# Kernel tuning notes

Hardware: AMD Instinct MI355X
Metric: run time of the kernel (lower is better)

The kernel has to match this reference:

```python
import jax, jax.numpy as jnp
import numpy as np

NUM_HEADS = 64
DIM = 128
# Rotation schedule: all (i, j) with i < j in row-major order, matching
# GivensRotationPerHead._create_rotation_indices. R = DIM*(DIM-1)//2 = 8128.
_II, _JJ = np.triu_indices(DIM, k=1)


def setup_inputs() -> dict:
    key = jax.random.key(0)
    thetas = jax.random.normal(key, (NUM_HEADS, _II.shape[0]), dtype=jnp.float32) * 0.01
    return {
        "thetas": thetas,
        "rot_i": jnp.asarray(_II, dtype=jnp.int32),
        "rot_j": jnp.asarray(_JJ, dtype=jnp.int32),
    }


def reference(thetas, rot_i, rot_j):
    # thetas: [H, R]; rot_i, rot_j: [R]
    H, R = thetas.shape
    dim = DIM
    # Precompute all cos/sin once ([R, H, 1]) instead of per-step trig.
    c = jnp.cos(thetas.T)[:, :, None]
    s = jnp.sin(thetas.T)[:, :, None]
    Q0 = jnp.broadcast_to(jnp.eye(dim, dtype=thetas.dtype), (H, dim, dim))

    def body(Q, xs):
        i, j, ci, si = xs
        Qi = Q[:, i, :]  # [H, dim]
        Qj = Q[:, j, :]  # [H, dim]
        Q = Q.at[:, i, :].set(ci * Qi + si * Qj)
        Q = Q.at[:, j, :].set(-si * Qi + ci * Qj)
        return Q, None

    Q, _ = jax.lax.scan(body, Q0, (rot_i, rot_j, c, s))
    return Q
```

## Files before the change

### kernel.cpp

```cpp
#include <hip/hip_runtime.h>

#define DIM 128
#define NHEAD 64
#define NROT 8128
#define NSEG28 28
#define MHEAD28 57344
#define KAC 168
#define CSROWS 64

typedef float f4 __attribute__((ext_vector_type(4)));
typedef short bf8 __attribute__((ext_vector_type(8)));
typedef unsigned short u16;

__device__ const int S_A0[NSEG28] = {0,0,0,8,8,8,16,16,16,24,24,32,32,40,40,
                                     48,48,56,56,64,64,72,80,88,96,104,112,120};
__device__ const int S_J0[NSEG28] = {8,56,104,16,64,112,24,72,120,32,80,40,88,48,96,
                                     56,104,64,112,72,120,80,88,96,104,112,120,128};
__device__ const int S_NJ[NSEG28] = {48,48,24,48,48,16,48,48,8,48,48,48,40,48,32,
                                     48,24,48,16,48,8,48,40,32,24,16,8,0};
__device__ const int S_OFF[NSEG28] = {0,3136,6272,7296,10432,13568,14144,17280,20416,
                                      20672,23808,26944,30080,32384,35520,37120,40256,
                                      41280,44416,44992,48128,48384,51520,53824,55424,
                                      56448,57024,57280};
__device__ const int S_INTRA[NSEG28] = {1,0,0,1,0,0,1,0,0,1,0,1,0,1,0,
                                        1,0,1,0,1,0,1,1,1,1,1,1,1};

__device__ __forceinline__ void sincos_poly(float x, float& sn, float& cn) {
    float x2 = x * x;
    sn = x * fmaf(x2, fmaf(x2, 8.33333333e-3f, -1.66666667e-1f), 1.0f);
    cn = fmaf(x2, fmaf(x2, 4.16666667e-2f, -0.5f), 1.0f);
}

__device__ __forceinline__ u16 f2bf(float v) {
    unsigned b = __float_as_uint(v);
    b += 0x7FFF + ((b >> 16) & 1);
    return (u16)(b >> 16);
}
__device__ __forceinline__ float bf2f(u16 h) {
    return __uint_as_float(((unsigned)h) << 16);
}

struct Row { f4 q0, q1, q2, q3; };

__device__ __forceinline__ void ldrow_u(Row& R, const float* p) {
    const f4* c4 = (const f4*)p;
    R.q0 = c4[0]; R.q1 = c4[1]; R.q2 = c4[2]; R.q3 = c4[3];
}

__device__ __forceinline__ float rowv(const Row& R, float p[8], float v) {
#define ROT2(c, s, T) { float pv = p[T]; float nv = fmaf((c), v, -((s) * pv)); \
                        p[T] = fmaf((s), v, (c) * pv); v = nv; }
    ROT2(R.q0.x, R.q0.y, 0) ROT2(R.q0.z, R.q0.w, 1)
    ROT2(R.q1.x, R.q1.y, 2) ROT2(R.q1.z, R.q1.w, 3)
    ROT2(R.q2.x, R.q2.y, 4) ROT2(R.q2.z, R.q2.w, 5)
    ROT2(R.q3.x, R.q3.y, 6) ROT2(R.q3.z, R.q3.w, 7)
#undef ROT2
    return v;
}

__device__ __forceinline__ void store_bf(u16* oh, u16* ol, int idx, float v, bool act) {
    u16 h = f2bf(v);
    u16 l = f2bf(v - bf2f(h));
    if (act) { oh[idx] = h; ol[idx] = l; }
}

__global__ __launch_bounds__(64, 1)
void chain28(const float* __restrict__ th_all,
             u16* __restrict__ MhW, u16* __restrict__ MlW)
{
    __shared__ __align__(16) float csx[56 + 48 * 16];

    const int lane = threadIdx.x;
    const int head = blockIdx.x & 63;
    const int s    = blockIdx.x >> 6;
    const int a0 = S_A0[s], j0 = S_J0[s], nj = S_NJ[s], n = 8 + nj;
    const bool intra = S_INTRA[s] != 0;
    const float* __restrict__ th = th_all + head * NROT;
    u16* __restrict__ oh = MhW + (size_t)head * MHEAD28 + S_OFF[s];
    u16* __restrict__ ol = MlW + (size_t)head * MHEAD28 + S_OFF[s];
    const bool cact = lane < n;
    const int ne = 8 * nj;
    const int d1 = j0 - a0 - 1;

    float thx[6];
    #pragma unroll
    for (int it = 0; it < 6; ++it) {
        if (it * 64 < ne) {
            int e = lane + it * 64;
            int t = e & 7, jr = e >> 3;
            int i = a0 + t;
            thx[it] = th[((i * (255 - i)) >> 1) + d1 - t + jr];
        }
    }
    float thi = 0.0f;
    if (intra && lane < 28) {
        int t1 = 0, rem = lane;
        while (rem >= 7 - t1) { rem -= 7 - t1; ++t1; }
        int t2 = t1 + 1 + rem;
        int i  = a0 + t1;
        thi = th[((i * (255 - i)) >> 1) + (t2 - t1 - 1)];
    }
    #pragma unroll
    for (int it = 0; it < 6; ++it) {
        if (it * 64 < ne) {
            int e = lane + it * 64;
            float sn, cn; sincos_poly(thx[it], sn, cn);
            csx[56 + 2 * e] = cn; csx[56 + 2 * e + 1] = sn;
        }
    }
    if (intra && lane < 28) {
        float sn, cn; sincos_poly(thi, sn, cn);
        csx[2 * lane] = cn; csx[2 * lane + 1] = sn;
    }
    __syncthreads();

    float p[8];
    #pragma unroll
    for (int t = 0; t < 8; ++t) p[t] = (lane == t) ? 1.0f : 0.0f;

    if (intra) {
        int idx = 0;
        #pragma unroll
        for (int t1 = 0; t1 < 8; ++t1) {
            #pragma unroll
            for (int t2 = t1 + 1; t2 < 8; ++t2) {
                float c = csx[2 * idx], sn = csx[2 * idx + 1];
                float pa = p[t1];
                p[t1] = fmaf(c, pa,    sn * p[t2]);
                p[t2] = fmaf(c, p[t2], -(sn * pa));
                ++idx;
            }
        }
    }

    if (nj > 0) {
        const float* cs = csx + 56;
        const int jv = lane - 8;
        Row A0, A1, B0, B1;
        ldrow_u(A0, cs); ldrow_u(A1, cs + 16);
        #pragma unroll 1
        for (int r = 0; r < nj; r += 4) {
            ldrow_u(B0, cs + 16 * (r + 2)); ldrow_u(B1, cs + 16 * (r + 3));
            float v0 = rowv(A0, p, (r     == jv) ? 1.0f : 0.0f);
            float v1 = rowv(A1, p, (r + 1 == jv) ? 1.0f : 0.0f);
            store_bf(oh, ol, (8 + r)     * n + lane, v0, cact);
            store_bf(oh, ol, (8 + r + 1) * n + lane, v1, cact);
            if (r + 4 < nj) { ldrow_u(A0, cs + 16 * (r + 4));
                              ldrow_u(A1, cs + 16 * (r + 5)); }
            float v2 = rowv(B0, p, (r + 2 == jv) ? 1.0f : 0.0f);
            float v3 = rowv(B1, p, (r + 3 == jv) ? 1.0f : 0.0f);
            store_bf(oh, ol, (8 + r + 2) * n + lane, v2, cact);
            store_bf(oh, ol, (8 + r + 3) * n + lane, v3, cact);
        }
    }

    #pragma unroll
    for (int t = 0; t < 8; ++t)
        store_bf(oh, ol, t * n + lane, p[t], cact);
}

__global__ __launch_bounds__(256, 1)
void compose4w(const u16* __restrict__ MhA, const u16* __restrict__ MlA,
               float* __restrict__ out)
{
    __shared__ u16 AhT[16][KAC];
    __shared__ u16 AlT[16][KAC];

    const int tid  = threadIdx.x;
    const int lane = tid & 63;
    const int w    = tid >> 6;
    const int head = blockIdx.x & 63;
    const int sl   = blockIdx.x >> 6;
    const int c0   = sl * 16;
    const u16* __restrict__ Mh = MhA + (size_t)head * MHEAD28;
    const u16* __restrict__ Ml = MlA + (size_t)head * MHEAD28;

    {
        int c = tid & 15, rr = tid >> 4, cg = c0 + c;
        for (int k = DIM + rr; k < KAC; k += 16) { AhT[c][k] = 0; AlT[c][k] = 0; }
        for (int r = rr; r < DIM; r += 16) {
            u16 h, l;
            if (r < 56 && cg < 56) { h = Mh[r * 56 + cg]; l = Ml[r * 56 + cg]; }
            else                   { h = (r == cg) ? (u16)0x3F80 : (u16)0; l = 0; }
            AhT[c][r] = h; AlT[c][r] = l;
        }
    }
    __syncthreads();

    const int fr = lane & 15;
    const int fk = (lane >> 4) * 8;
    const int r4 = (lane >> 4) * 4;
    const int ro = 16 * w;

    auto ldM = [&](int s, bf8& ah0, bf8& al0, bf8& ah1, bf8& al1) {
        const int n = 8 + S_NJ[s];
        const u16* __restrict__ Msh = Mh + S_OFF[s];
        const u16* __restrict__ Msl = Ml + S_OFF[s];
        const int rA  = ro + fr;
        const int rAc = (rA < n) ? rA : (n - 1);
        const int kc0 = (fk <= n - 8) ? fk : (n - 8);
        const int kx  = 32 + fk;
        const int kc1 = (kx <= n - 8) ? kx : (n - 8);
        ah0 = *(const bf8*)&Msh[(size_t)rAc * n + kc0];
        al0 = *(const bf8*)&Msl[(size_t)rAc * n + kc0];
        ah1 = *(const bf8*)&Msh[(size_t)rAc * n + kc1];
        al1 = *(const bf8*)&Msl[(size_t)rAc * n + kc1];
    };

    bf8 cah0, cal0, cah1, cal1;
    bf8 nah0, nal0, nah1, nal1;
    ldM(1, cah0, cal0, cah1, cal1);

    #pragma unroll 1
    for (int s = 1; s < NSEG28; ++s) {
        const int a0 = S_A0[s], j0 = S_J0[s], n = 8 + S_NJ[s];

        const int kk0 = fk, kx = 32 + fk;
        const int b0 = (kk0 < 8) ? (a0 + kk0) : ((kk0 < n) ? (j0 + kk0 - 8) : 128);
        const int b1 = (kx  < 8) ? (a0 + kx)  : ((kx  < n) ? (j0 + kx  - 8) : 128);
        bf8 bh0 = *(const bf8*)&AhT[fr][b0];
        bf8 bl0 = *(const bf8*)&AlT[fr][b0];
        bf8 bh1 = *(const bf8*)&AhT[fr][b1];
        bf8 bl1 = *(const bf8*)&AlT[fr][b1];

        if (s + 1 < NSEG28) ldM(s + 1, nah0, nal0, nah1, nal1);

        const bool act = ro < n;
        f4 acc = {0, 0, 0, 0};
        if (act) {
            acc = __builtin_amdgcn_mfma_f32_16x16x32_bf16(cah0, bh0, acc, 0, 0, 0);
            acc = __builtin_amdgcn_mfma_f32_16x16x32_bf16(cah0, bl0, acc, 0, 0, 0);
            acc = __builtin_amdgcn_mfma_f32_16x16x32_bf16(cal0, bh0, acc, 0, 0, 0);
            acc = __builtin_amdgcn_mfma_f32_16x16x32_bf16(cal0, bl0, acc, 0, 0, 0);
            acc = __builtin_amdgcn_mfma_f32_16x16x32_bf16(cah1, bh1, acc, 0, 0, 0);
            acc = __builtin_amdgcn_mfma_f32_16x16x32_bf16(cah1, bl1, acc, 0, 0, 0);
            acc = __builtin_amdgcn_mfma_f32_16x16x32_bf16(cal1, bh1, acc, 0, 0, 0);
            acc = __builtin_amdgcn_mfma_f32_16x16x32_bf16(cal1, bl1, acc, 0, 0, 0);
        }

        __syncthreads();

        const int rowq = ro + r4;
        if (act && rowq < n) {
            const int rg = (rowq < 8) ? (a0 + rowq) : (j0 + rowq - 8);
            float v0 = acc[0], v1 = acc[1], v2 = acc[2], v3 = acc[3];
            u16 h0 = f2bf(v0), h1 = f2bf(v1), h2 = f2bf(v2), h3 = f2bf(v3);
            u16 l0 = f2bf(v0 - bf2f(h0)), l1 = f2bf(v1 - bf2f(h1));
            u16 l2 = f2bf(v2 - bf2f(h2)), l3 = f2bf(v3 - bf2f(h3));
            ushort4 hv; hv.x = h0; hv.y = h1; hv.z = h2; hv.w = h3;
            ushort4 lv; lv.x = l0; lv.y = l1; lv.z = l2; lv.w = l3;
            *(ushort4*)&AhT[fr][rg] = hv;
            *(ushort4*)&AlT[fr][rg] = lv;
        }
        __syncthreads();

        cah0 = nah0; cal0 = nal0; cah1 = nah1; cal1 = nal1;
    }

    {
        int c = tid & 15, rr = tid >> 4;
        float* o = out + (size_t)head * (DIM * DIM) + c0;
        for (int r = rr; r < DIM; r += 16)
            o[r * DIM + c] = bf2f(AhT[c][r]) + bf2f(AlT[c][r]);
    }
}

#define QA(r, c) Q[(r)][ (c) ^ ((r) & 31) ]
#define ROTP(c, s, T, v) { float pt = p[T]; p[T] = fmaf((c), pt, (s) * (v)); \
                           (v) = fmaf((c), (v), -((s) * pt)); }
__device__ __forceinline__ void rot8q(const Row& r, float p[8], float& v) {
    ROTP(r.q0.x, r.q0.y, 0, v) ROTP(r.q0.z, r.q0.w, 1, v)
    ROTP(r.q1.x, r.q1.y, 2, v) ROTP(r.q1.z, r.q1.w, 3, v)
    ROTP(r.q2.x, r.q2.y, 4, v) ROTP(r.q2.z, r.q2.w, 5, v)
    ROTP(r.q3.x, r.q3.y, 6, v) ROTP(r.q3.z, r.q3.w, 7, v)
}

__global__ __launch_bounds__(64, 1)
void chain_mono(const float* __restrict__ th_all, float* __restrict__ outp)
{
    __shared__ float Q[DIM][64];
    __shared__ __align__(16) float csx[56 + CSROWS * 16];

    const int lane = threadIdx.x;
    const int head = blockIdx.x & 63;
    const int cb   = blockIdx.x >> 6;
    const int col_glob = cb * 64 + lane;
    const float* __restrict__ th = th_all + head * NROT;

    for (int r = 0; r < DIM; ++r)
        QA(r, lane) = (r == col_glob) ? 1.0f : 0.0f;

    #pragma unroll 1
    for (int g = 0; g < 16; ++g) {
        const int a0  = 8 * g;
        const int ntr = 120 - a0;
        float p[8];
        const int nsub = (ntr > CSROWS) ? 2 : 1;
        #pragma unroll 1
        for (int sub = 0; sub < nsub; ++sub) {
            const int r0 = sub * CSROWS;
            const int nr = (ntr - r0) < CSROWS ? (ntr - r0) : CSROWS;
            const int ne = 8 * nr;
            __syncthreads();
            float thx[8];
            #pragma unroll
            for (int it = 0; it < 8; ++it) {
                if (it * 64 < ne) {
                    int e = lane + it * 64;
                    int t = e & 7, jr = r0 + (e >> 3);
                    int i = a0 + t;
                    thx[it] = th[((i * (255 - i)) >> 1) + jr + 7 - t];
                }
            }
            float thi = 0.0f;
            if (sub == 0 && lane < 28) {
                int t1 = 0, rem = lane;
                while (rem >= 7 - t1) { rem -= 7 - t1; ++t1; }
                int t2 = t1 + 1 + rem;
                int i  = a0 + t1;
                thi = th[((i * (255 - i)) >> 1) + (t2 - t1 - 1)];
            }
            #pragma unroll
            for (int it = 0; it < 8; ++it) {
                if (it * 64 < ne) {
                    int e = lane + it * 64;
                    float sn, cn; sincos_poly(thx[it], sn, cn);
                    csx[56 + 2 * e] = cn; csx[56 + 2 * e + 1] = sn;
                }
            }
            if (sub == 0 && lane < 28) {
                float sn, cn; sincos_poly(thi, sn, cn);
                csx[2 * lane] = cn; csx[2 * lane + 1] = sn;
            }
            __syncthreads();

            if (sub == 0) {
                #pragma unroll
                for (int t = 0; t < 8; ++t) p[t] = QA(a0 + t, lane);
                int idx = 0;
                #pragma unroll
                for (int t1 = 0; t1 < 8; ++t1) {
                    #pragma unroll
                    for (int t2 = t1 + 1; t2 < 8; ++t2) {
                        float c = csx[2 * idx], sn = csx[2 * idx + 1];
                        float pa = p[t1];
                        p[t1] = fmaf(c, pa,    sn * p[t2]);
                        p[t2] = fmaf(c, p[t2], -(sn * pa));
                        ++idx;
                    }
                }
            }
            if (nr > 0) {
                const float* cs = csx + 56;
                const int base = a0 + 8 + r0;
                Row A0, A1, B0, B1;
                float vA0, vA1, vB0, vB1;
                auto ldpair = [&](Row& R, float& v, int r) {
                    ldrow_u(R, cs + 16 * r);
                    v = QA(base + r, lane);
                };
                ldpair(A0, vA0, 0); ldpair(A1, vA1, 1);
                #pragma unroll 1
                for (int r = 0; r < nr; r += 4) {
                    ldpair(B0, vB0, r + 2); ldpair(B1, vB1, r + 3);
                    rot8q(A0, p, vA0); rot8q(A1, p, vA1);
                    QA(base + r, lane)     = vA0;
                    QA(base + r + 1, lane) = vA1;
                    if (r + 4 < nr) { ldpair(A0, vA0, r + 4); ldpair(A1, vA1, r + 5); }
                    rot8q(B0, p, vB0); rot8q(B1, p, vB1);
                    QA(base + r + 2, lane) = vB0;
                    QA(base + r + 3, lane) = vB1;
                }
            }
        }
        #pragma unroll
        for (int t = 0; t < 8; ++t) QA(a0 + t, lane) = p[t];
    }

    __syncthreads();
    float* o = outp + head * (DIM * DIM) + col_glob;
    #pragma unroll 1
    for (int r = 0; r < DIM; ++r) o[r * DIM] = QA(r, lane);
}

extern "C" void kernel_launch(void* const* d_in, const int* in_sizes, int n_in,
                              void* d_out, int out_size, void* d_ws, size_t ws_size,
                              hipStream_t stream) {
    const float* thetas = (const float*)d_in[0];
    float* out = (float*)d_out;
    const size_t need = (size_t)NHEAD * MHEAD28 * 2 * sizeof(u16);

    if (ws_size >= need) {
        u16* MhW = (u16*)d_ws;
        u16* MlW = MhW + (size_t)NHEAD * MHEAD28;
        chain28<<<dim3(NSEG28 * NHEAD), dim3(64), 0, stream>>>(thetas, MhW, MlW);
        compose4w<<<dim3(8 * NHEAD), dim3(256), 0, stream>>>(MhW, MlW, out);
    } else {
        chain_mono<<<dim3(2 * NHEAD), dim3(64), 0, stream>>>(thetas, out);
    }
}
```

Baseline: 40.96 us.

## Coarsen Givens chain segmentation from 28 eight-row segments to 7 thirty-two-row segments

```diff
diff --git a/kernel.cpp b/kernel.cpp
--- a/kernel.cpp
+++ b/kernel.cpp
@@ -3,8 +3,8 @@
 #define DIM 128
 #define NHEAD 64
 #define NROT 8128
-#define NSEG28 28
-#define MHEAD28 57344
+#define NSEG7 7
+#define MHEAD7 25600
 #define KAC 168
 #define CSROWS 64
 
@@ -12,18 +12,12 @@
 typedef short bf8 __attribute__((ext_vector_type(8)));
 typedef unsigned short u16;
 
-__device__ const int S_A0[NSEG28] = {0,0,0,8,8,8,16,16,16,24,24,32,32,40,40,
-                                     48,48,56,56,64,64,72,80,88,96,104,112,120};
-__device__ const int S_J0[NSEG28] = {8,56,104,16,64,112,24,72,120,32,80,40,88,48,96,
-                                     56,104,64,112,72,120,80,88,96,104,112,120,128};
-__device__ const int S_NJ[NSEG28] = {48,48,24,48,48,16,48,48,8,48,48,48,40,48,32,
-                                     48,24,48,16,48,8,48,40,32,24,16,8,0};
-__device__ const int S_OFF[NSEG28] = {0,3136,6272,7296,10432,13568,14144,17280,20416,
-                                      20672,23808,26944,30080,32384,35520,37120,40256,
-                                      41280,44416,44992,48128,48384,51520,53824,55424,
-                                      56448,57024,57280};
-__device__ const int S_INTRA[NSEG28] = {1,0,0,1,0,0,1,0,0,1,0,1,0,1,0,
-                                        1,0,1,0,1,0,1,1,1,1,1,1,1};
+__device__ const int C_A0[NSEG7]   = {0,0,0,32,32,64,96};
+__device__ const int C_J0[NSEG7]   = {32,64,96,64,96,96,128};
+__device__ const int C_NJ[NSEG7]   = {32,32,32,32,32,32,0};
+__device__ const int C_N[NSEG7]    = {64,64,64,64,64,64,32};
+__device__ const int C_OFF[NSEG7]  = {0,4096,8192,12288,16384,20480,24576};
+__device__ const int C_INTRA[NSEG7]= {1,0,0,1,0,1,1};
 
 __device__ __forceinline__ void sincos_poly(float x, float& sn, float& cn) {
     float x2 = x * x;
@@ -40,22 +34,8 @@
     return __uint_as_float(((unsigned)h) << 16);
 }
 
-struct Row { f4 q0, q1, q2, q3; };
-
-__device__ __forceinline__ void ldrow_u(Row& R, const float* p) {
-    const f4* c4 = (const f4*)p;
-    R.q0 = c4[0]; R.q1 = c4[1]; R.q2 = c4[2]; R.q3 = c4[3];
-}
-
-__device__ __forceinline__ float rowv(const Row& R, float p[8], float v) {
-#define ROT2(c, s, T) { float pv = p[T]; float nv = fmaf((c), v, -((s) * pv)); \
-                        p[T] = fmaf((s), v, (c) * pv); v = nv; }
-    ROT2(R.q0.x, R.q0.y, 0) ROT2(R.q0.z, R.q0.w, 1)
-    ROT2(R.q1.x, R.q1.y, 2) ROT2(R.q1.z, R.q1.w, 3)
-    ROT2(R.q2.x, R.q2.y, 4) ROT2(R.q2.z, R.q2.w, 5)
-    ROT2(R.q3.x, R.q3.y, 6) ROT2(R.q3.z, R.q3.w, 7)
-#undef ROT2
-    return v;
+__device__ __forceinline__ int tri_base(int i) {
+    return (i * (2 * DIM - 1 - i)) >> 1;
 }
 
 __device__ __forceinline__ void store_bf(u16* oh, u16* ol, int idx, float v, bool act) {
@@ -65,66 +45,75 @@
 }
 
 __global__ __launch_bounds__(64, 1)
-void chain28(const float* __restrict__ th_all,
-             u16* __restrict__ MhW, u16* __restrict__ MlW)
+void chain7(const float* __restrict__ th_all,
+            u16* __restrict__ MhW, u16* __restrict__ MlW)
 {
-    __shared__ __align__(16) float csx[56 + 48 * 16];
+    __shared__ __align__(16) float csx[992 + 32 * 64];
 
     const int lane = threadIdx.x;
     const int head = blockIdx.x & 63;
     const int s    = blockIdx.x >> 6;
-    const int a0 = S_A0[s], j0 = S_J0[s], nj = S_NJ[s], n = 8 + nj;
-    const bool intra = S_INTRA[s] != 0;
+    const int a0 = C_A0[s], j0 = C_J0[s], nj = C_NJ[s], n = C_N[s];
+    const bool intra = C_INTRA[s] != 0;
     const float* __restrict__ th = th_all + head * NROT;
-    u16* __restrict__ oh = MhW + (size_t)head * MHEAD28 + S_OFF[s];
-    u16* __restrict__ ol = MlW + (size_t)head * MHEAD28 + S_OFF[s];
+    u16* __restrict__ oh = MhW + (size_t)head * MHEAD7 + C_OFF[s];
+    u16* __restrict__ ol = MlW + (size_t)head * MHEAD7 + C_OFF[s];
     const bool cact = lane < n;
-    const int ne = 8 * nj;
+    const int ne = 32 * nj;
     const int d1 = j0 - a0 - 1;
 
-    float thx[6];
-    #pragma unroll
-    for (int it = 0; it < 6; ++it) {
+    float thx[16];
+    #pragma unroll
+    for (int it = 0; it < 16; ++it) {
         if (it * 64 < ne) {
             int e = lane + it * 64;
-            int t = e & 7, jr = e >> 3;
-            int i = a0 + t;
-            thx[it] = th[((i * (255 - i)) >> 1) + d1 - t + jr];
-        }
-    }
-    float thi = 0.0f;
-    if (intra && lane < 28) {
-        int t1 = 0, rem = lane;
-        while (rem >= 7 - t1) { rem -= 7 - t1; ++t1; }
-        int t2 = t1 + 1 + rem;
-        int i  = a0 + t1;
-        thi = th[((i * (255 - i)) >> 1) + (t2 - t1 - 1)];
-    }
-    #pragma unroll
-    for (int it = 0; it < 6; ++it) {
+            int t = e & 31, r = e >> 5;
+            thx[it] = th[tri_base(a0 + t) + d1 + r - t];
+        }
+    }
+    float thi[8];
+    #pragma unroll
+    for (int it = 0; it < 8; ++it) {
+        int e = lane + it * 64;
+        if (intra && e < 496) {
+            int t1 = 0, rem = e;
+            while (rem >= 31 - t1) { rem -= 31 - t1; ++t1; }
+            int t2 = t1 + 1 + rem;
+            thi[it] = th[tri_base(a0 + t1) + (t2 - t1 - 1)];
+        }
+    }
+    #pragma unroll
+    for (int it = 0; it < 16; ++it) {
         if (it * 64 < ne) {
             int e = lane + it * 64;
             float sn, cn; sincos_poly(thx[it], sn, cn);
-            csx[56 + 2 * e] = cn; csx[56 + 2 * e + 1] = sn;
-        }
-    }
-    if (intra && lane < 28) {
-        float sn, cn; sincos_poly(thi, sn, cn);
-        csx[2 * lane] = cn; csx[2 * lane + 1] = sn;
+            csx[992 + 2 * e] = cn; csx[992 + 2 * e + 1] = sn;
+        }
+    }
+    #pragma unroll
+    for (int it = 0; it < 8; ++it) {
+        int e = lane + it * 64;
+        if (intra && e < 496) {
+            float sn, cn; sincos_poly(thi[it], sn, cn);
+            csx[2 * e] = cn; csx[2 * e + 1] = sn;
+        }
     }
     __syncthreads();
 
-    float p[8];
-    #pragma unroll
-    for (int t = 0; t < 8; ++t) p[t] = (lane == t) ? 1.0f : 0.0f;
+    float p[32];
+    #pragma unroll
+    for (int t = 0; t < 32; ++t) p[t] = (lane == t) ? 1.0f : 0.0f;
 
     if (intra) {
+        f4 cc;
         int idx = 0;
         #pragma unroll
-        for (int t1 = 0; t1 < 8; ++t1) {
-            #pragma unroll
-            for (int t2 = t1 + 1; t2 < 8; ++t2) {
-                float c = csx[2 * idx], sn = csx[2 * idx + 1];
+        for (int t1 = 0; t1 < 31; ++t1) {
+            #pragma unroll
+            for (int t2 = t1 + 1; t2 < 32; ++t2) {
+                float c, sn;
+                if ((idx & 1) == 0) { cc = *(const f4*)&csx[2 * idx]; c = cc.x; sn = cc.y; }
+                else                { c = cc.z; sn = cc.w; }
                 float pa = p[t1];
                 p[t1] = fmaf(c, pa,    sn * p[t2]);
                 p[t2] = fmaf(c, p[t2], -(sn * pa));
@@ -134,34 +123,35 @@
     }
 
     if (nj > 0) {
-        const float* cs = csx + 56;
-        const int jv = lane - 8;
-        Row A0, A1, B0, B1;
-        ldrow_u(A0, cs); ldrow_u(A1, cs + 16);
-        #pragma unroll 1
-        for (int r = 0; r < nj; r += 4) {
-            ldrow_u(B0, cs + 16 * (r + 2)); ldrow_u(B1, cs + 16 * (r + 3));
-            float v0 = rowv(A0, p, (r     == jv) ? 1.0f : 0.0f);
-            float v1 = rowv(A1, p, (r + 1 == jv) ? 1.0f : 0.0f);
-            store_bf(oh, ol, (8 + r)     * n + lane, v0, cact);
-            store_bf(oh, ol, (8 + r + 1) * n + lane, v1, cact);
-            if (r + 4 < nj) { ldrow_u(A0, cs + 16 * (r + 4));
-                              ldrow_u(A1, cs + 16 * (r + 5)); }
-            float v2 = rowv(B0, p, (r + 2 == jv) ? 1.0f : 0.0f);
-            float v3 = rowv(B1, p, (r + 3 == jv) ? 1.0f : 0.0f);
-            store_bf(oh, ol, (8 + r + 2) * n + lane, v2, cact);
-            store_bf(oh, ol, (8 + r + 3) * n + lane, v3, cact);
-        }
-    }
-
-    #pragma unroll
-    for (int t = 0; t < 8; ++t)
+        const float* cs = csx + 992;
+        const int jv = lane - 32;
+        #pragma unroll 2
+        for (int r = 0; r < nj; ++r) {
+            const f4* c4 = (const f4*)(cs + r * 64);
+            f4 q[16];
+            #pragma unroll
+            for (int i = 0; i < 16; ++i) q[i] = c4[i];
+            float v = (r == jv) ? 1.0f : 0.0f;
+            #pragma unroll
+            for (int t = 0; t < 32; t += 2) {
+                f4 qq = q[t >> 1];
+                { float pv = p[t];     float nv = fmaf(qq.x, v, -(qq.y * pv));
+                  p[t]     = fmaf(qq.y, v, qq.x * pv); v = nv; }
+                { float pv = p[t + 1]; float nv = fmaf(qq.z, v, -(qq.w * pv));
+                  p[t + 1] = fmaf(qq.w, v, qq.z * pv); v = nv; }
+            }
+            store_bf(oh, ol, (32 + r) * n + lane, v, cact);
+        }
+    }
+
+    #pragma unroll
+    for (int t = 0; t < 32; ++t)
         store_bf(oh, ol, t * n + lane, p[t], cact);
 }
 
 __global__ __launch_bounds__(256, 1)
-void compose4w(const u16* __restrict__ MhA, const u16* __restrict__ MlA,
-               float* __restrict__ out)
+void compose7(const u16* __restrict__ MhA, const u16* __restrict__ MlA,
+              float* __restrict__ out)
 {
     __shared__ u16 AhT[16][KAC];
     __shared__ u16 AlT[16][KAC];
@@ -172,15 +162,15 @@
     const int head = blockIdx.x & 63;
     const int sl   = blockIdx.x >> 6;
     const int c0   = sl * 16;
-    const u16* __restrict__ Mh = MhA + (size_t)head * MHEAD28;
-    const u16* __restrict__ Ml = MlA + (size_t)head * MHEAD28;
+    const u16* __restrict__ Mh = MhA + (size_t)head * MHEAD7;
+    const u16* __restrict__ Ml = MlA + (size_t)head * MHEAD7;
 
     {
         int c = tid & 15, rr = tid >> 4, cg = c0 + c;
         for (int k = DIM + rr; k < KAC; k += 16) { AhT[c][k] = 0; AlT[c][k] = 0; }
         for (int r = rr; r < DIM; r += 16) {
             u16 h, l;
-            if (r < 56 && cg < 56) { h = Mh[r * 56 + cg]; l = Ml[r * 56 + cg]; }
+            if (r < 64 && cg < 64) { h = Mh[r * 64 + cg]; l = Ml[r * 64 + cg]; }
             else                   { h = (r == cg) ? (u16)0x3F80 : (u16)0; l = 0; }
             AhT[c][r] = h; AlT[c][r] = l;
         }
@@ -193,37 +183,35 @@
     const int ro = 16 * w;
 
     auto ldM = [&](int s, bf8& ah0, bf8& al0, bf8& ah1, bf8& al1) {
-        const int n = 8 + S_NJ[s];
-        const u16* __restrict__ Msh = Mh + S_OFF[s];
-        const u16* __restrict__ Msl = Ml + S_OFF[s];
+        const int n = C_N[s];
+        const u16* __restrict__ Msh = Mh + C_OFF[s];
+        const u16* __restrict__ Msl = Ml + C_OFF[s];
         const int rA  = ro + fr;
         const int rAc = (rA < n) ? rA : (n - 1);
-        const int kc0 = (fk <= n - 8) ? fk : (n - 8);
         const int kx  = 32 + fk;
         const int kc1 = (kx <= n - 8) ? kx : (n - 8);
-        ah0 = *(const bf8*)&Msh[(size_t)rAc * n + kc0];
-        al0 = *(const bf8*)&Msl[(size_t)rAc * n + kc0];
+        ah0 = *(const bf8*)&Msh[(size_t)rAc * n + fk];
+        al0 = *(const bf8*)&Msl[(size_t)rAc * n + fk];
         ah1 = *(const bf8*)&Msh[(size_t)rAc * n + kc1];
         al1 = *(const bf8*)&Msl[(size_t)rAc * n + kc1];
     };
 
-    bf8 cah0, cal0, cah1, cal1;
-    bf8 nah0, nal0, nah1, nal1;
+    bf8 cah0, cal0, cah1, cal1, nah0, nal0, nah1, nal1;
     ldM(1, cah0, cal0, cah1, cal1);
 
     #pragma unroll 1
-    for (int s = 1; s < NSEG28; ++s) {
-        const int a0 = S_A0[s], j0 = S_J0[s], n = 8 + S_NJ[s];
-
-        const int kk0 = fk, kx = 32 + fk;
-        const int b0 = (kk0 < 8) ? (a0 + kk0) : ((kk0 < n) ? (j0 + kk0 - 8) : 128);
-        const int b1 = (kx  < 8) ? (a0 + kx)  : ((kx  < n) ? (j0 + kx  - 8) : 128);
+    for (int s = 1; s < NSEG7; ++s) {
+        const int a0 = C_A0[s], j0 = C_J0[s], n = C_N[s];
+
+        const int kx = 32 + fk;
+        const int b0 = a0 + fk;
+        const int b1 = (kx < n) ? (j0 + fk) : 128;
         bf8 bh0 = *(const bf8*)&AhT[fr][b0];
         bf8 bl0 = *(const bf8*)&AlT[fr][b0];
         bf8 bh1 = *(const bf8*)&AhT[fr][b1];
         bf8 bl1 = *(const bf8*)&AlT[fr][b1];
 
-        if (s + 1 < NSEG28) ldM(s + 1, nah0, nal0, nah1, nal1);
+        if (s + 1 < NSEG7) ldM(s + 1, nah0, nal0, nah1, nal1);
 
         const bool act = ro < n;
         f4 acc = {0, 0, 0, 0};
@@ -242,7 +230,7 @@
 
         const int rowq = ro + r4;
         if (act && rowq < n) {
-            const int rg = (rowq < 8) ? (a0 + rowq) : (j0 + rowq - 8);
+            const int rg = (rowq < 32) ? (a0 + rowq) : (j0 + rowq - 32);
             float v0 = acc[0], v1 = acc[1], v2 = acc[2], v3 = acc[3];
             u16 h0 = f2bf(v0), h1 = f2bf(v1), h2 = f2bf(v2), h3 = f2bf(v3);
             u16 l0 = f2bf(v0 - bf2f(h0)), l1 = f2bf(v1 - bf2f(h1));
@@ -265,10 +253,15 @@
     }
 }
 
+struct Row8 { f4 q0, q1, q2, q3; };
+__device__ __forceinline__ void ldrow_u(Row8& R, const float* p) {
+    const f4* c4 = (const f4*)p;
+    R.q0 = c4[0]; R.q1 = c4[1]; R.q2 = c4[2]; R.q3 = c4[3];
+}
 #define QA(r, c) Q[(r)][ (c) ^ ((r) & 31) ]
 #define ROTP(c, s, T, v) { float pt = p[T]; p[T] = fmaf((c), pt, (s) * (v)); \
                            (v) = fmaf((c), (v), -((s) * pt)); }
-__device__ __forceinline__ void rot8q(const Row& r, float p[8], float& v) {
+__device__ __forceinline__ void rot8q(const Row8& r, float p[8], float& v) {
     ROTP(r.q0.x, r.q0.y, 0, v) ROTP(r.q0.z, r.q0.w, 1, v)
     ROTP(r.q1.x, r.q1.y, 2, v) ROTP(r.q1.z, r.q1.w, 3, v)
     ROTP(r.q2.x, r.q2.y, 4, v) ROTP(r.q2.z, r.q2.w, 5, v)
@@ -308,8 +301,7 @@
                 if (it * 64 < ne) {
                     int e = lane + it * 64;
                     int t = e & 7, jr = r0 + (e >> 3);
-                    int i = a0 + t;
-                    thx[it] = th[((i * (255 - i)) >> 1) + jr + 7 - t];
+                    thx[it] = th[tri_base(a0 + t) + jr + 7 - t];
                 }
             }
             float thi = 0.0f;
@@ -317,8 +309,7 @@
                 int t1 = 0, rem = lane;
                 while (rem >= 7 - t1) { rem -= 7 - t1; ++t1; }
                 int t2 = t1 + 1 + rem;
-                int i  = a0 + t1;
-                thi = th[((i * (255 - i)) >> 1) + (t2 - t1 - 1)];
+                thi = th[tri_base(a0 + t1) + (t2 - t1 - 1)];
             }
             #pragma unroll
             for (int it = 0; it < 8; ++it) {
@@ -353,9 +344,9 @@
             if (nr > 0) {
                 const float* cs = csx + 56;
                 const int base = a0 + 8 + r0;
-                Row A0, A1, B0, B1;
+                Row8 A0, A1, B0, B1;
                 float vA0, vA1, vB0, vB1;
-                auto ldpair = [&](Row& R, float& v, int r) {
+                auto ldpair = [&](Row8& R, float& v, int r) {
                     ldrow_u(R, cs + 16 * r);
                     v = QA(base + r, lane);
                 };
@@ -388,13 +379,13 @@
                               hipStream_t stream) {
     const float* thetas = (const float*)d_in[0];
     float* out = (float*)d_out;
-    const size_t need = (size_t)NHEAD * MHEAD28 * 2 * sizeof(u16);
+    const size_t need = (size_t)NHEAD * MHEAD7 * 2 * sizeof(u16);
 
     if (ws_size >= need) {
         u16* MhW = (u16*)d_ws;
-        u16* MlW = MhW + (size_t)NHEAD * MHEAD28;
-        chain28<<<dim3(NSEG28 * NHEAD), dim3(64), 0, stream>>>(thetas, MhW, MlW);
-        compose4w<<<dim3(8 * NHEAD), dim3(256), 0, stream>>>(MhW, MlW, out);
+        u16* MlW = MhW + (size_t)NHEAD * MHEAD7;
+        chain7<<<dim3(NSEG7 * NHEAD), dim3(64), 0, stream>>>(thetas, MhW, MlW);
+        compose7<<<dim3(8 * NHEAD), dim3(256), 0, stream>>>(MhW, MlW, out);
     } else {
         chain_mono<<<dim3(2 * NHEAD), dim3(64), 0, stream>>>(thetas, out);
     }
```

Result: faster. 39.87 us (-2.7%).
